# Performance work log

Measured on AMD Instinct MI355X. Metric: run time of the kernel, lower is better.

The kernel has to match this reference:

```python
import jax, jax.numpy as jnp
import numpy as np

N_NODES = 50000
N_FEAT = 32
HIDDEN = 64
K_HOPS = 3
N_EDGES = 800000
BN_EPS = 1e-5


def setup_inputs() -> dict:
    key = jax.random.key(0)
    ks = jax.random.split(key, 16)
    x = jax.random.normal(ks[0], (N_NODES, N_FEAT), jnp.float32)
    edge_index = jax.random.randint(ks[1], (2, N_EDGES), 0, N_NODES, jnp.int32)
    edge_weight = jax.random.uniform(ks[2], (N_EDGES,), jnp.float32, minval=0.1, maxval=1.0)
    fin = N_FEAT + HIDDEN  # DCRNN cell concatenates [X, H]
    s = 1.0 / np.sqrt(fin)
    Wz = jax.random.uniform(ks[3], (2, K_HOPS, fin, HIDDEN), jnp.float32, -s, s)
    Wr = jax.random.uniform(ks[4], (2, K_HOPS, fin, HIDDEN), jnp.float32, -s, s)
    Wh = jax.random.uniform(ks[5], (2, K_HOPS, fin, HIDDEN), jnp.float32, -s, s)
    bz = jax.random.uniform(ks[6], (HIDDEN,), jnp.float32, -s, s)
    br = jax.random.uniform(ks[7], (HIDDEN,), jnp.float32, -s, s)
    bh = jax.random.uniform(ks[8], (HIDDEN,), jnp.float32, -s, s)
    g = 1.0 / np.sqrt(HIDDEN)
    gcn_w = jax.random.uniform(ks[9], (HIDDEN, HIDDEN), jnp.float32, -g, g)
    gcn_b = jax.random.uniform(ks[10], (HIDDEN,), jnp.float32, -g, g)
    bn_gamma = jnp.ones((HIDDEN,), jnp.float32)
    bn_beta = jnp.zeros((HIDDEN,), jnp.float32)
    lin_w = jax.random.uniform(ks[11], (HIDDEN, 1), jnp.float32, -g, g)
    lin_b = jax.random.uniform(ks[12], (1,), jnp.float32, -g, g)
    return dict(x=x, edge_index=edge_index, edge_weight=edge_weight,
                Wz=Wz, bz=bz, Wr=Wr, br=br, Wh=Wh, bh=bh,
                gcn_w=gcn_w, gcn_b=gcn_b, bn_gamma=bn_gamma, bn_beta=bn_beta,
                lin_w=lin_w, lin_b=lin_b)


def _dconv(X, W, b, row, col, ew, do_inv, di_inv, n):
    # Diffusion conv: H = sum_k T_out^k(X) @ W[0,k] + T_in^k(X) @ W[1,k] + b
    # T_out: propagate along edges (source -> target), out-degree normalized
    # T_in : propagate along reversed edges, in-degree normalized
    H = X @ W[0, 0] + X @ W[1, 0]
    Tx_o = X
    Tx_i = X
    w_out = (ew * do_inv[row])[:, None]  # [E,1]
    w_in = (ew * di_inv[col])[:, None]   # [E,1]
    for k in range(1, W.shape[1]):
        Tx_o = jax.ops.segment_sum(w_out * Tx_o[row], col, num_segments=n)
        Tx_i = jax.ops.segment_sum(w_in * Tx_i[col], row, num_segments=n)
        H = H + Tx_o @ W[0, k] + Tx_i @ W[1, k]
    return H + b


def reference(x, edge_index, edge_weight, Wz, bz, Wr, br, Wh, bh,
              gcn_w, gcn_b, bn_gamma, bn_beta, lin_w, lin_b):
    n = x.shape[0]
    row, col = edge_index[0], edge_index[1]
    # weighted degrees (as in DConv's dense-adjacency degree computation)
    deg_out = jax.ops.segment_sum(edge_weight, row, num_segments=n)
    deg_in = jax.ops.segment_sum(edge_weight, col, num_segments=n)
    do_inv = jnp.where(deg_out > 0, 1.0 / deg_out, 0.0)
    di_inv = jnp.where(deg_in > 0, 1.0 / deg_in, 0.0)

    # --- DCRNN cell (GRU with diffusion convs), hidden state starts at zero ---
    H0 = jnp.zeros((n, Wz.shape[-1]), x.dtype)
    XH = jnp.concatenate([x, H0], axis=1)
    Z = jax.nn.sigmoid(_dconv(XH, Wz, bz, row, col, edge_weight, do_inv, di_inv, n))
    R = jax.nn.sigmoid(_dconv(XH, Wr, br, row, col, edge_weight, do_inv, di_inv, n))
    XHR = jnp.concatenate([x, H0 * R], axis=1)
    H_tilde = jnp.tanh(_dconv(XHR, Wh, bh, row, col, edge_weight, do_inv, di_inv, n))
    H = Z * H0 + (1.0 - Z) * H_tilde  # [N, HIDDEN]

    # --- GCNConv(H, edge_index) with unit edge weights + self loops, sym norm ---
    xw = H @ gcn_w
    ones_e = jnp.ones((row.shape[0],), x.dtype)
    deg = jax.ops.segment_sum(ones_e, col, num_segments=n) + 1.0  # + self loop
    dis = jnp.where(deg > 0, jax.lax.rsqrt(deg), 0.0)
    norm = (dis[row] * dis[col])[:, None]
    y = jax.ops.segment_sum(norm * xw[row], col, num_segments=n) + (dis * dis)[:, None] * xw
    y = y + gcn_b

    # ReLU -> BatchNorm1d (batch statistics, biased var) -> Dropout(identity/eval) -> Linear
    y = jax.nn.relu(y)
    mean = jnp.mean(y, axis=0)
    var = jnp.mean(jnp.square(y - mean), axis=0)
    y = (y - mean) * jax.lax.rsqrt(var + BN_EPS) * bn_gamma + bn_beta
    out = y @ lin_w + lin_b  # [N, 1]
    return out
```

## Files before the change

### kernel.cpp

```cpp
#include <hip/hip_runtime.h>
#include <hip/hip_fp16.h>
#include <math.h>


#define BN_EPS 1e-5f
#define CAPB 6
#define CAP  64
#define ITEMS 2048
#define KI 8
#define REGCAP 5120

typedef _Float16 v8h __attribute__((ext_vector_type(8)));
typedef float v4f __attribute__((ext_vector_type(4)));

__global__ __launch_bounds__(256) void k_sort1(
    const int* __restrict__ row, const int* __restrict__ col,
    const float* __restrict__ ew,
    unsigned long long* __restrict__ bufC, unsigned long long* __restrict__ bufR,
    unsigned* __restrict__ gcnt, int E, int nbk, int reg) {
    __shared__ unsigned hist[256], scanb[256], cur[256], runb[256];
    __shared__ unsigned long long outb[ITEMS];
    int t = threadIdx.x;
    int s = (blockIdx.x >= nbk) ? 1 : 0;
    int blk = blockIdx.x - s * nbk;
    int e0 = blk * ITEMS;
    int vcnt = E - e0; if (vcnt > ITEMS) vcnt = ITEMS;
    hist[t] = 0;
    __syncthreads();
    for (int k = 0; k < KI; ++k) {
        int e = e0 + k * 256 + t;
        if (e < E) {
            int key = s ? row[e] : col[e];
            atomicAdd(&hist[key >> 8], 1u);
        }
    }
    __syncthreads();
    scanb[t] = hist[t];
    __syncthreads();
    for (int off = 1; off < 256; off <<= 1) {
        unsigned v = (t >= off) ? scanb[t - off] : 0u;
        __syncthreads();
        scanb[t] += v;
        __syncthreads();
    }
    unsigned excl = scanb[t] - hist[t];
    __syncthreads();
    scanb[t] = excl;
    cur[t] = excl;
    runb[t] = (unsigned)(t * reg) + atomicAdd(&gcnt[s * 256 + t], hist[t]);
    __syncthreads();
    for (int k = 0; k < KI; ++k) {
        int e = e0 + k * 256 + t;
        if (e < E) {
            int key, oth;
            if (s) { key = row[e]; oth = col[e]; }
            else   { key = col[e]; oth = row[e]; }
            unsigned hw = (unsigned)__half_as_ushort(__float2half(ew[e]));
            unsigned long long it = ((unsigned long long)(unsigned)key << 32)
                                  | ((unsigned)oth << 16) | hw;
            unsigned r = atomicAdd(&cur[key >> 8], 1u);
            outb[r] = it;
        }
    }
    __syncthreads();
    unsigned long long* buf = s ? bufR : bufC;
    for (int k = 0; k < KI; ++k) {
        int idx = k * 256 + t;
        if (idx < vcnt) {
            unsigned long long it = outb[idx];
            unsigned d = (unsigned)(it >> 40) & 255u;
            buf[(size_t)runb[d] + ((unsigned)idx - scanb[d])] = it;
        }
    }
}

__global__ __launch_bounds__(256) void k_sort2(
    const unsigned long long* __restrict__ buf, const unsigned* __restrict__ gcnt,
    unsigned* __restrict__ ent, int* __restrict__ cnt, int N, int reg) {
    __shared__ unsigned hist[256], scanb[256], cur[256];
    __shared__ unsigned outp[REGCAP];
    __shared__ unsigned char outl[REGCAP];
    int t = threadIdx.x;
    int d0 = blockIdx.x;
    const unsigned long long* src = buf + (size_t)d0 * reg;
    int cin = (int)gcnt[d0]; if (cin > REGCAP) cin = REGCAP;
    hist[t] = 0;
    __syncthreads();
    for (int i = t; i < cin; i += 256) {
        unsigned l = (unsigned)(src[i] >> 32) & 255u;
        atomicAdd(&hist[l], 1u);
    }
    __syncthreads();
    scanb[t] = hist[t];
    __syncthreads();
    for (int off = 1; off < 256; off <<= 1) {
        unsigned v = (t >= off) ? scanb[t - off] : 0u;
        __syncthreads();
        scanb[t] += v;
        __syncthreads();
    }
    unsigned excl = scanb[t] - hist[t];
    __syncthreads();
    scanb[t] = excl;
    cur[t] = excl;
    int node0 = d0 << 8;
    if (node0 + t < N) cnt[node0 + t] = (int)hist[t];
    __syncthreads();
    for (int i = t; i < cin; i += 256) {
        unsigned long long it = src[i];
        unsigned l = (unsigned)(it >> 32) & 255u;
        unsigned r = atomicAdd(&cur[l], 1u);
        outp[r] = (unsigned)it;
        outl[r] = (unsigned char)l;
    }
    __syncthreads();
    for (int i = t; i < cin; i += 256) {
        unsigned l = outl[i];
        int slot = i - (int)scanb[l];
        int node = node0 + (int)l;
        if (slot < CAP && node < N)
            ent[((size_t)node << CAPB) + slot] = outp[i];
    }
}

__device__ inline float ent_w(unsigned e) {
    return __half2float(__ushort_as_half((unsigned short)(e & 0xffffu)));
}

__global__ void k_degs(const unsigned* __restrict__ ent_col, const unsigned* __restrict__ ent_row,
                       const int* __restrict__ cnt_col, const int* __restrict__ cnt_row,
                       float* __restrict__ do_inv, float* __restrict__ di_inv,
                       float* __restrict__ dis, int N) {
    int i = blockIdx.x * blockDim.x + threadIdx.x;
    if (i >= N) return;
    float s = 0.f;
    int c = min(cnt_row[i], CAP);
    const unsigned* er = ent_row + ((size_t)i << CAPB);
    for (int j = 0; j < c; ++j) s += ent_w(er[j]);
    do_inv[i] = s > 0.f ? 1.f / s : 0.f;
    s = 0.f;
    c = min(cnt_col[i], CAP);
    const unsigned* ec = ent_col + ((size_t)i << CAPB);
    for (int j = 0; j < c; ++j) s += ent_w(ec[j]);
    di_inv[i] = s > 0.f ? 1.f / s : 0.f;
    dis[i] = rsqrtf((float)cnt_col[i] + 1.0f);
}

__global__ void k_cvt_x(const float* __restrict__ xf, __half* __restrict__ xh, int n2) {
    int t = blockIdx.x * blockDim.x + threadIdx.x;
    if (t >= n2) return;
    float2 v = *(const float2*)(xf + 2 * (size_t)t);
    __half2 h; h.x = __float2half(v.x); h.y = __float2half(v.y);
    *(__half2*)(xh + 2 * (size_t)t) = h;
}

__global__ void k_hop(const unsigned* __restrict__ ent_col, const unsigned* __restrict__ ent_row,
                      const int* __restrict__ cnt_col, const int* __restrict__ cnt_row,
                      const __half* __restrict__ So, const __half* __restrict__ Si,
                      const float* __restrict__ do_inv, const float* __restrict__ di_inv,
                      __half* __restrict__ Do, __half* __restrict__ Di, int N) {
    int t = blockIdx.x * blockDim.x + threadIdx.x;
    int f = t & 31;
    int p = t >> 5;
    if (p >= 2 * N) return;
    const unsigned* ent; const __half* S; const float* inv; __half* D;
    int d, cnt;
    if (p < N) { d = p;     ent = ent_col; S = So; inv = do_inv; D = Do; cnt = min(cnt_col[d], CAP); }
    else       { d = p - N; ent = ent_row; S = Si; inv = di_inv; D = Di; cnt = min(cnt_row[d], CAP); }
    ent += ((size_t)d << CAPB);
    float acc = 0.f;
    int j = 0;
    for (; j + 7 < cnt; j += 8) {
        unsigned e0 = ent[j],     e1 = ent[j + 1], e2 = ent[j + 2], e3 = ent[j + 3];
        unsigned e4 = ent[j + 4], e5 = ent[j + 5], e6 = ent[j + 6], e7 = ent[j + 7];
        int s0 = e0 >> 16, s1 = e1 >> 16, s2 = e2 >> 16, s3 = e3 >> 16;
        int s4 = e4 >> 16, s5 = e5 >> 16, s6 = e6 >> 16, s7 = e7 >> 16;
        float i0 = inv[s0], i1 = inv[s1], i2 = inv[s2], i3 = inv[s3];
        float i4 = inv[s4], i5 = inv[s5], i6 = inv[s6], i7 = inv[s7];
        float v0 = __half2float(S[(size_t)s0 * 32 + f]);
        float v1 = __half2float(S[(size_t)s1 * 32 + f]);
        float v2 = __half2float(S[(size_t)s2 * 32 + f]);
        float v3 = __half2float(S[(size_t)s3 * 32 + f]);
        float v4 = __half2float(S[(size_t)s4 * 32 + f]);
        float v5 = __half2float(S[(size_t)s5 * 32 + f]);
        float v6 = __half2float(S[(size_t)s6 * 32 + f]);
        float v7 = __half2float(S[(size_t)s7 * 32 + f]);
        acc += ent_w(e0) * i0 * v0 + ent_w(e1) * i1 * v1
             + ent_w(e2) * i2 * v2 + ent_w(e3) * i3 * v3
             + ent_w(e4) * i4 * v4 + ent_w(e5) * i5 * v5
             + ent_w(e6) * i6 * v6 + ent_w(e7) * i7 * v7;
    }
    for (; j + 3 < cnt; j += 4) {
        unsigned e0 = ent[j],     e1 = ent[j + 1];
        unsigned e2 = ent[j + 2], e3 = ent[j + 3];
        int s0 = e0 >> 16, s1 = e1 >> 16, s2 = e2 >> 16, s3 = e3 >> 16;
        float i0 = inv[s0], i1 = inv[s1], i2 = inv[s2], i3 = inv[s3];
        float v0 = __half2float(S[(size_t)s0 * 32 + f]);
        float v1 = __half2float(S[(size_t)s1 * 32 + f]);
        float v2 = __half2float(S[(size_t)s2 * 32 + f]);
        float v3 = __half2float(S[(size_t)s3 * 32 + f]);
        acc += ent_w(e0) * i0 * v0 + ent_w(e1) * i1 * v1
             + ent_w(e2) * i2 * v2 + ent_w(e3) * i3 * v3;
    }
    for (; j < cnt; ++j) {
        unsigned e0 = ent[j];
        int s0 = e0 >> 16;
        acc += ent_w(e0) * inv[s0] * __half2float(S[(size_t)s0 * 32 + f]);
    }
    D[(size_t)d * 32 + f] = __float2half(acc);
}

__global__ void k_wprep(const float* __restrict__ Wz, const float* __restrict__ Wh,
                        const float* __restrict__ gcn_w,
                        __half* __restrict__ wzT, __half* __restrict__ whT,
                        __half* __restrict__ gwT) {
    int t = blockIdx.x * blockDim.x + threadIdx.x;
    if (t < 64 * 160) {
        int c = t / 160, k = t % 160;
        int blk = k >> 5, r = k & 31;
        float vz, vh;
        if (blk == 0) {
            vz = Wz[r * 64 + c] + Wz[(288 + r) * 64 + c];
            vh = Wh[r * 64 + c] + Wh[(288 + r) * 64 + c];
        } else {
            int kk = (blk + 1) >> 1, dd = (blk + 1) & 1;
            int off = ((dd * 3 + kk) * 96 + r) * 64 + c;
            vz = Wz[off]; vh = Wh[off];
        }
        wzT[t] = __float2half(vz);
        whT[t] = __float2half(vh);
    }
    if (t < 64 * 64) {
        int c = t >> 6, k = t & 63;
        gwT[t] = __float2half(gcn_w[k * 64 + c]);
    }
}

__device__ inline v8h ldh8(const __half* p) { return *(const v8h*)p; }

__global__ __launch_bounds__(256) void k_zh_mfma(
    const __half* __restrict__ xh, const __half* __restrict__ t1o,
    const __half* __restrict__ t1i, const __half* __restrict__ t2o,
    const __half* __restrict__ t2i,
    const __half* __restrict__ wzT, const __half* __restrict__ whT,
    const __half* __restrict__ gwT,
    const float* __restrict__ bz, const float* __restrict__ bh,
    const float* __restrict__ dis, float* __restrict__ xws, int N) {
    __shared__ _Float16 Hl[16 * 72];
    int lane = threadIdx.x & 63;
    int wv = threadIdx.x >> 6;
    int q = lane >> 4, m = lane & 15;
    int c = wv * 16 + m;
    int ko = q * 8;

    const __half* wz = wzT + c * 160 + ko;
    const __half* wh = whT + c * 160 + ko;
    v8h bz0 = ldh8(wz),       bh0 = ldh8(wh);
    v8h bz1 = ldh8(wz + 32),  bh1 = ldh8(wh + 32);
    v8h bz2 = ldh8(wz + 64),  bh2 = ldh8(wh + 64);
    v8h bz3 = ldh8(wz + 96),  bh3 = ldh8(wh + 96);
    v8h bz4 = ldh8(wz + 128), bh4 = ldh8(wh + 128);
    v8h g0 = ldh8(gwT + c * 64 + ko);
    v8h g1 = ldh8(gwT + c * 64 + 32 + ko);
    float bzc = bz[c], bhc = bh[c];

    int T = (N + 15) >> 4;
    for (int t = blockIdx.x; t < T; t += gridDim.x) {
        int n0 = t << 4;
        int nn = n0 + m; if (nn > N - 1) nn = N - 1;
        size_t off = (size_t)nn * 32 + ko;
        v8h a0 = ldh8(xh + off);
        v8h a1 = ldh8(t1o + off);
        v8h a2 = ldh8(t1i + off);
        v8h a3 = ldh8(t2o + off);
        v8h a4 = ldh8(t2i + off);
        v4f az = {0.f, 0.f, 0.f, 0.f}, ah = {0.f, 0.f, 0.f, 0.f};
        az = __builtin_amdgcn_mfma_f32_16x16x32_f16(a0, bz0, az, 0, 0, 0);
        ah = __builtin_amdgcn_mfma_f32_16x16x32_f16(a0, bh0, ah, 0, 0, 0);
        az = __builtin_amdgcn_mfma_f32_16x16x32_f16(a1, bz1, az, 0, 0, 0);
        ah = __builtin_amdgcn_mfma_f32_16x16x32_f16(a1, bh1, ah, 0, 0, 0);
        az = __builtin_amdgcn_mfma_f32_16x16x32_f16(a2, bz2, az, 0, 0, 0);
        ah = __builtin_amdgcn_mfma_f32_16x16x32_f16(a2, bh2, ah, 0, 0, 0);
        az = __builtin_amdgcn_mfma_f32_16x16x32_f16(a3, bz3, az, 0, 0, 0);
        ah = __builtin_amdgcn_mfma_f32_16x16x32_f16(a3, bh3, ah, 0, 0, 0);
        az = __builtin_amdgcn_mfma_f32_16x16x32_f16(a4, bz4, az, 0, 0, 0);
        ah = __builtin_amdgcn_mfma_f32_16x16x32_f16(a4, bh4, ah, 0, 0, 0);

#pragma unroll
        for (int i = 0; i < 4; ++i) {
            float zv = 1.f / (1.f + expf(-(az[i] + bzc)));
            float hv = (1.f - zv) * tanhf(ah[i] + bhc);
            Hl[(q * 4 + i) * 72 + c] = (_Float16)hv;
        }
        __syncthreads();
        v8h ha0 = *(const v8h*)&Hl[m * 72 + ko];
        v8h ha1 = *(const v8h*)&Hl[m * 72 + 32 + ko];
        v4f bacc = {0.f, 0.f, 0.f, 0.f};
        bacc = __builtin_amdgcn_mfma_f32_16x16x32_f16(ha0, g0, bacc, 0, 0, 0);
        bacc = __builtin_amdgcn_mfma_f32_16x16x32_f16(ha1, g1, bacc, 0, 0, 0);
#pragma unroll
        for (int i = 0; i < 4; ++i) {
            int node = n0 + q * 4 + i;
            if (node < N) xws[(size_t)node * 64 + c] = dis[node] * bacc[i];
        }
        __syncthreads();
    }
}

__global__ __launch_bounds__(256) void k_gcn16(
    const unsigned* __restrict__ ent_col, const int* __restrict__ cnt_col,
    const float* __restrict__ dis, const float* __restrict__ xws,
    const float* __restrict__ gcn_b,
    float* __restrict__ y, float* __restrict__ stats, int N) {
    __shared__ float red[2][256];
    int t = threadIdx.x;
    int ch = t & 15;
    int grp = t >> 4;
    int s = blockIdx.x & 3;
    int cg = s * 16 + ch;
    float bl = gcn_b[cg];
    int bi = blockIdx.x >> 2;
    int nblk = gridDim.x >> 2;
    float sa = 0.f, s2a = 0.f;
    for (int d = bi * 16 + grp; d < N; d += nblk * 16) {
        float sum = xws[(size_t)d * 64 + cg];
        const unsigned* ent = ent_col + ((size_t)d << CAPB);
        int cnt = min(cnt_col[d], CAP);
        int j = 0;
        for (; j + 7 < cnt; j += 8) {
            unsigned e0 = ent[j],     e1 = ent[j + 1], e2 = ent[j + 2], e3 = ent[j + 3];
            unsigned e4 = ent[j + 4], e5 = ent[j + 5], e6 = ent[j + 6], e7 = ent[j + 7];
            float v0 = xws[(size_t)(e0 >> 16) * 64 + cg];
            float v1 = xws[(size_t)(e1 >> 16) * 64 + cg];
            float v2 = xws[(size_t)(e2 >> 16) * 64 + cg];
            float v3 = xws[(size_t)(e3 >> 16) * 64 + cg];
            float v4 = xws[(size_t)(e4 >> 16) * 64 + cg];
            float v5 = xws[(size_t)(e5 >> 16) * 64 + cg];
            float v6 = xws[(size_t)(e6 >> 16) * 64 + cg];
            float v7 = xws[(size_t)(e7 >> 16) * 64 + cg];
            sum += (v0 + v1 + v2 + v3) + (v4 + v5 + v6 + v7);
        }
        for (; j + 3 < cnt; j += 4) {
            unsigned e0 = ent[j],     e1 = ent[j + 1];
            unsigned e2 = ent[j + 2], e3 = ent[j + 3];
            float v0 = xws[(size_t)(e0 >> 16) * 64 + cg];
            float v1 = xws[(size_t)(e1 >> 16) * 64 + cg];
            float v2 = xws[(size_t)(e2 >> 16) * 64 + cg];
            float v3 = xws[(size_t)(e3 >> 16) * 64 + cg];
            sum += v0 + v1 + v2 + v3;
        }
        for (; j < cnt; ++j) {
            unsigned e0 = ent[j];
            sum += xws[(size_t)(e0 >> 16) * 64 + cg];
        }
        float v = dis[d] * sum + bl;
        v = v > 0.f ? v : 0.f;
        y[(size_t)d * 64 + cg] = v;
        sa += v; s2a += v * v;
    }
    red[0][t] = sa;
    red[1][t] = s2a;
    __syncthreads();
    if (t < 16) {
        float ts = 0.f, ts2 = 0.f;
        for (int k = t; k < 256; k += 16) { ts += red[0][k]; ts2 += red[1][k]; }
        atomicAdd(&stats[s * 16 + t], ts);
        atomicAdd(&stats[64 + s * 16 + t], ts2);
    }
}

__global__ void k_final(const float* __restrict__ y, const float* __restrict__ stats,
                        const float* __restrict__ gma, const float* __restrict__ bta,
                        const float* __restrict__ lw, const float* __restrict__ lb,
                        float* __restrict__ out, int N) {
    int lane = threadIdx.x & 63;
    int wave = (blockIdx.x * blockDim.x + threadIdx.x) >> 6;
    if (wave >= N) return;
    float invN = 1.0f / (float)N;
    float mean = stats[lane] * invN;
    float var  = stats[64 + lane] * invN - mean * mean;
    float istd = rsqrtf(var + BN_EPS);
    float v = y[(size_t)wave * 64 + lane];
    float t = (v - mean) * istd * gma[lane] + bta[lane];
    float p = t * lw[lane];
    for (int off = 32; off > 0; off >>= 1)
        p += __shfl_down(p, off, 64);
    if (lane == 0) out[wave] = p + lb[0];
}

extern "C" void kernel_launch(void* const* d_in, const int* in_sizes, int n_in,
                              void* d_out, int out_size, void* d_ws, size_t ws_size,
                              hipStream_t stream) {
    const float* x     = (const float*)d_in[0];
    const int*   ei    = (const int*)d_in[1];
    const float* ew    = (const float*)d_in[2];
    const float* Wz    = (const float*)d_in[3];
    const float* bz    = (const float*)d_in[4];
    const float* Wh    = (const float*)d_in[7];
    const float* bhv   = (const float*)d_in[8];
    const float* gcn_w = (const float*)d_in[9];
    const float* gcn_b = (const float*)d_in[10];
    const float* gma   = (const float*)d_in[11];
    const float* bta   = (const float*)d_in[12];
    const float* lw    = (const float*)d_in[13];
    const float* lb    = (const float*)d_in[14];
    float* out = (float*)d_out;

    const int N = in_sizes[0] / 32;
    const int E = in_sizes[2];
    const int* row = ei;
    const int* col = ei + E;

    float* ws      = (float*)d_ws;
    int*   cnt_col = (int*)ws;
    int*   cnt_row = (int*)(ws + (size_t)N);
    unsigned* gcnt = (unsigned*)(ws + 2 * (size_t)N);
    float* stats   = ws + 2 * (size_t)N + 512;
    size_t Z0      = 2 * (size_t)N + 640;
    float* dis     = ws + Z0;
    float* do_inv  = ws + Z0 + (size_t)N;
    float* di_inv  = ws + Z0 + 2 * (size_t)N;
    __half* xh     = (__half*)(ws + Z0 + 3 * (size_t)N);
    __half* txo1   = (__half*)(ws + Z0 + 19 * (size_t)N);
    __half* txi1   = (__half*)(ws + Z0 + 35 * (size_t)N);
    __half* txo2   = (__half*)(ws + Z0 + 51 * (size_t)N);
    __half* txi2   = (__half*)(ws + Z0 + 67 * (size_t)N);
    unsigned* ent_col = (unsigned*)(ws + Z0 + 83 * (size_t)N);
    unsigned* ent_row = ent_col + ((size_t)N << CAPB);
    float* xws     = (float*)ent_row;
    float* ybuf    = (float*)txo1;
    __half* wzT    = (__half*)(ws + Z0 + 211 * (size_t)N);
    __half* whT    = wzT + 64 * 160;
    __half* gwT    = whT + 64 * 160;

    unsigned long long* bufC = (unsigned long long*)ent_row;
    unsigned long long* bufR = (unsigned long long*)txo1;

    size_t zero_bytes = (2 * (size_t)N + 640) * sizeof(float);
    hipMemsetAsync(d_ws, 0, zero_bytes, stream);

    int NB = (N + 255) / 256;
    int nbk = (E + ITEMS - 1) / ITEMS;
    int ndig = (N + 255) / 256;
    k_cvt_x<<<(16 * N + 255) / 256, 256, 0, stream>>>(x, xh, 16 * N);
    k_wprep<<<40, 256, 0, stream>>>(Wz, Wh, gcn_w, wzT, whT, gwT);
    k_sort1<<<2 * nbk, 256, 0, stream>>>(row, col, ew, bufC, bufR, gcnt, E, nbk, REGCAP);
    k_sort2<<<ndig, 256, 0, stream>>>(bufC, gcnt,       ent_col, cnt_col, N, REGCAP);
    k_sort2<<<ndig, 256, 0, stream>>>(bufR, gcnt + 256, ent_row, cnt_row, N, REGCAP);
    k_degs <<<NB, 256, 0, stream>>>(ent_col, ent_row, cnt_col, cnt_row,
                                    do_inv, di_inv, dis, N);

    int bhop = (2 * N * 32 + 255) / 256;
    k_hop<<<bhop, 256, 0, stream>>>(ent_col, ent_row, cnt_col, cnt_row,
                                    xh, xh, do_inv, di_inv, txo1, txi1, N);
    k_hop<<<bhop, 256, 0, stream>>>(ent_col, ent_row, cnt_col, cnt_row,
                                    txo1, txi1, do_inv, di_inv, txo2, txi2, N);

    k_zh_mfma<<<1024, 256, 0, stream>>>(xh, txo1, txi1, txo2, txi2,
                                        wzT, whT, gwT, bz, bhv, dis, xws, N);

    k_gcn16<<<1600, 256, 0, stream>>>(ent_col, cnt_col, dis, xws,
                                      gcn_b, ybuf, stats, N);
    k_final<<<(N + 3) / 4, 256, 0, stream>>>(ybuf, stats, gma, bta, lw, lb, out, N);
}
```

Measured before the change: 291.0 us.

## Aggregate GCN neighbors before the weight matmul, gathering fp16 hidden states

```diff
diff --git a/kernel.cpp b/kernel.cpp
--- a/kernel.cpp
+++ b/kernel.cpp
@@ -243,10 +243,8 @@
     const __half* __restrict__ t1i, const __half* __restrict__ t2o,
     const __half* __restrict__ t2i,
     const __half* __restrict__ wzT, const __half* __restrict__ whT,
-    const __half* __restrict__ gwT,
     const float* __restrict__ bz, const float* __restrict__ bh,
-    const float* __restrict__ dis, float* __restrict__ xws, int N) {
-    __shared__ _Float16 Hl[16 * 72];
+    const float* __restrict__ dis, __half* __restrict__ Hd, int N) {
     int lane = threadIdx.x & 63;
     int wv = threadIdx.x >> 6;
     int q = lane >> 4, m = lane & 15;
@@ -260,8 +258,6 @@
     v8h bz2 = ldh8(wz + 64),  bh2 = ldh8(wh + 64);
     v8h bz3 = ldh8(wz + 96),  bh3 = ldh8(wh + 96);
     v8h bz4 = ldh8(wz + 128), bh4 = ldh8(wh + 128);
-    v8h g0 = ldh8(gwT + c * 64 + ko);
-    v8h g1 = ldh8(gwT + c * 64 + 32 + ko);
     float bzc = bz[c], bhc = bh[c];
 
     int T = (N + 15) >> 4;
@@ -290,82 +286,104 @@
         for (int i = 0; i < 4; ++i) {
             float zv = 1.f / (1.f + expf(-(az[i] + bzc)));
             float hv = (1.f - zv) * tanhf(ah[i] + bhc);
-            Hl[(q * 4 + i) * 72 + c] = (_Float16)hv;
-        }
-        __syncthreads();
-        v8h ha0 = *(const v8h*)&Hl[m * 72 + ko];
-        v8h ha1 = *(const v8h*)&Hl[m * 72 + 32 + ko];
-        v4f bacc = {0.f, 0.f, 0.f, 0.f};
-        bacc = __builtin_amdgcn_mfma_f32_16x16x32_f16(ha0, g0, bacc, 0, 0, 0);
-        bacc = __builtin_amdgcn_mfma_f32_16x16x32_f16(ha1, g1, bacc, 0, 0, 0);
+            int node = n0 + q * 4 + i;
+            if (node < N) Hd[(size_t)node * 64 + c] = __float2half(dis[node] * hv);
+        }
+    }
+}
+
+__global__ __launch_bounds__(256) void k_agg(
+    const unsigned* __restrict__ ent_col, const int* __restrict__ cnt_col,
+    const float* __restrict__ dis, const __half* __restrict__ Hd,
+    float* __restrict__ P, int N) {
+    int t = blockIdx.x * blockDim.x + threadIdx.x;
+    int ch = t & 63;
+    int d = t >> 6;
+    if (d >= N) return;
+    const unsigned* ent = ent_col + ((size_t)d << CAPB);
+    int cnt = min(cnt_col[d], CAP);
+    float acc = __half2float(Hd[(size_t)d * 64 + ch]);
+    int j = 0;
+    for (; j + 7 < cnt; j += 8) {
+        unsigned e0 = ent[j],     e1 = ent[j + 1], e2 = ent[j + 2], e3 = ent[j + 3];
+        unsigned e4 = ent[j + 4], e5 = ent[j + 5], e6 = ent[j + 6], e7 = ent[j + 7];
+        float v0 = __half2float(Hd[(size_t)(e0 >> 16) * 64 + ch]);
+        float v1 = __half2float(Hd[(size_t)(e1 >> 16) * 64 + ch]);
+        float v2 = __half2float(Hd[(size_t)(e2 >> 16) * 64 + ch]);
+        float v3 = __half2float(Hd[(size_t)(e3 >> 16) * 64 + ch]);
+        float v4 = __half2float(Hd[(size_t)(e4 >> 16) * 64 + ch]);
+        float v5 = __half2float(Hd[(size_t)(e5 >> 16) * 64 + ch]);
+        float v6 = __half2float(Hd[(size_t)(e6 >> 16) * 64 + ch]);
+        float v7 = __half2float(Hd[(size_t)(e7 >> 16) * 64 + ch]);
+        acc += (v0 + v1 + v2 + v3) + (v4 + v5 + v6 + v7);
+    }
+    for (; j + 3 < cnt; j += 4) {
+        unsigned e0 = ent[j],     e1 = ent[j + 1];
+        unsigned e2 = ent[j + 2], e3 = ent[j + 3];
+        float v0 = __half2float(Hd[(size_t)(e0 >> 16) * 64 + ch]);
+        float v1 = __half2float(Hd[(size_t)(e1 >> 16) * 64 + ch]);
+        float v2 = __half2float(Hd[(size_t)(e2 >> 16) * 64 + ch]);
+        float v3 = __half2float(Hd[(size_t)(e3 >> 16) * 64 + ch]);
+        acc += v0 + v1 + v2 + v3;
+    }
+    for (; j < cnt; ++j) {
+        acc += __half2float(Hd[(size_t)(ent[j] >> 16) * 64 + ch]);
+    }
+    P[(size_t)d * 64 + ch] = dis[d] * acc;
+}
+
+__global__ __launch_bounds__(256) void k_gcn2(
+    const float* __restrict__ P, const __half* __restrict__ gwT,
+    const float* __restrict__ gcn_b,
+    float* __restrict__ y, float* __restrict__ stats, int N) {
+    __shared__ float red[2][256];
+    int lane = threadIdx.x & 63;
+    int wv = threadIdx.x >> 6;
+    int q = lane >> 4, m = lane & 15;
+    int c = wv * 16 + m;
+    int ko = q * 8;
+    v8h g0 = ldh8(gwT + c * 64 + ko);
+    v8h g1 = ldh8(gwT + c * 64 + 32 + ko);
+    float bl = gcn_b[c];
+    float sa = 0.f, s2a = 0.f;
+    int T = (N + 15) >> 4;
+    for (int t = blockIdx.x; t < T; t += gridDim.x) {
+        int n0 = t << 4;
+        int nn = n0 + m; if (nn > N - 1) nn = N - 1;
+        const float* pr = P + (size_t)nn * 64;
+        v4f p0 = *(const v4f*)(pr + ko);
+        v4f p1 = *(const v4f*)(pr + ko + 4);
+        v4f p2 = *(const v4f*)(pr + 32 + ko);
+        v4f p3 = *(const v4f*)(pr + 32 + ko + 4);
+        v8h a0, a1;
+#pragma unroll
+        for (int j = 0; j < 4; ++j) {
+            a0[j] = (_Float16)p0[j]; a0[4 + j] = (_Float16)p1[j];
+            a1[j] = (_Float16)p2[j]; a1[4 + j] = (_Float16)p3[j];
+        }
+        v4f acc = {0.f, 0.f, 0.f, 0.f};
+        acc = __builtin_amdgcn_mfma_f32_16x16x32_f16(a0, g0, acc, 0, 0, 0);
+        acc = __builtin_amdgcn_mfma_f32_16x16x32_f16(a1, g1, acc, 0, 0, 0);
 #pragma unroll
         for (int i = 0; i < 4; ++i) {
             int node = n0 + q * 4 + i;
-            if (node < N) xws[(size_t)node * 64 + c] = dis[node] * bacc[i];
-        }
-        __syncthreads();
-    }
-}
-
-__global__ __launch_bounds__(256) void k_gcn16(
-    const unsigned* __restrict__ ent_col, const int* __restrict__ cnt_col,
-    const float* __restrict__ dis, const float* __restrict__ xws,
-    const float* __restrict__ gcn_b,
-    float* __restrict__ y, float* __restrict__ stats, int N) {
-    __shared__ float red[2][256];
-    int t = threadIdx.x;
-    int ch = t & 15;
-    int grp = t >> 4;
-    int s = blockIdx.x & 3;
-    int cg = s * 16 + ch;
-    float bl = gcn_b[cg];
-    int bi = blockIdx.x >> 2;
-    int nblk = gridDim.x >> 2;
-    float sa = 0.f, s2a = 0.f;
-    for (int d = bi * 16 + grp; d < N; d += nblk * 16) {
-        float sum = xws[(size_t)d * 64 + cg];
-        const unsigned* ent = ent_col + ((size_t)d << CAPB);
-        int cnt = min(cnt_col[d], CAP);
-        int j = 0;
-        for (; j + 7 < cnt; j += 8) {
-            unsigned e0 = ent[j],     e1 = ent[j + 1], e2 = ent[j + 2], e3 = ent[j + 3];
-            unsigned e4 = ent[j + 4], e5 = ent[j + 5], e6 = ent[j + 6], e7 = ent[j + 7];
-            float v0 = xws[(size_t)(e0 >> 16) * 64 + cg];
-            float v1 = xws[(size_t)(e1 >> 16) * 64 + cg];
-            float v2 = xws[(size_t)(e2 >> 16) * 64 + cg];
-            float v3 = xws[(size_t)(e3 >> 16) * 64 + cg];
-            float v4 = xws[(size_t)(e4 >> 16) * 64 + cg];
-            float v5 = xws[(size_t)(e5 >> 16) * 64 + cg];
-            float v6 = xws[(size_t)(e6 >> 16) * 64 + cg];
-            float v7 = xws[(size_t)(e7 >> 16) * 64 + cg];
-            sum += (v0 + v1 + v2 + v3) + (v4 + v5 + v6 + v7);
-        }
-        for (; j + 3 < cnt; j += 4) {
-            unsigned e0 = ent[j],     e1 = ent[j + 1];
-            unsigned e2 = ent[j + 2], e3 = ent[j + 3];
-            float v0 = xws[(size_t)(e0 >> 16) * 64 + cg];
-            float v1 = xws[(size_t)(e1 >> 16) * 64 + cg];
-            float v2 = xws[(size_t)(e2 >> 16) * 64 + cg];
-            float v3 = xws[(size_t)(e3 >> 16) * 64 + cg];
-            sum += v0 + v1 + v2 + v3;
-        }
-        for (; j < cnt; ++j) {
-            unsigned e0 = ent[j];
-            sum += xws[(size_t)(e0 >> 16) * 64 + cg];
-        }
-        float v = dis[d] * sum + bl;
-        v = v > 0.f ? v : 0.f;
-        y[(size_t)d * 64 + cg] = v;
-        sa += v; s2a += v * v;
-    }
-    red[0][t] = sa;
-    red[1][t] = s2a;
-    __syncthreads();
-    if (t < 16) {
-        float ts = 0.f, ts2 = 0.f;
-        for (int k = t; k < 256; k += 16) { ts += red[0][k]; ts2 += red[1][k]; }
-        atomicAdd(&stats[s * 16 + t], ts);
-        atomicAdd(&stats[64 + s * 16 + t], ts2);
+            if (node < N) {
+                float v = acc[i] + bl;
+                v = v > 0.f ? v : 0.f;
+                y[(size_t)node * 64 + c] = v;
+                sa += v; s2a += v * v;
+            }
+        }
+    }
+    red[0][threadIdx.x] = sa;
+    red[1][threadIdx.x] = s2a;
+    __syncthreads();
+    if (q == 0) {
+        int t0 = threadIdx.x;
+        float ts  = red[0][t0] + red[0][t0 + 16] + red[0][t0 + 32] + red[0][t0 + 48];
+        float ts2 = red[1][t0] + red[1][t0 + 16] + red[1][t0 + 32] + red[1][t0 + 48];
+        atomicAdd(&stats[c], ts);
+        atomicAdd(&stats[64 + c], ts2);
     }
 }
 
@@ -427,14 +445,15 @@
     __half* txi2   = (__half*)(ws + Z0 + 67 * (size_t)N);
     unsigned* ent_col = (unsigned*)(ws + Z0 + 83 * (size_t)N);
     unsigned* ent_row = ent_col + ((size_t)N << CAPB);
-    float* xws     = (float*)ent_row;
-    float* ybuf    = (float*)txo1;
     __half* wzT    = (__half*)(ws + Z0 + 211 * (size_t)N);
     __half* whT    = wzT + 64 * 160;
     __half* gwT    = whT + 64 * 160;
 
     unsigned long long* bufC = (unsigned long long*)ent_row;
     unsigned long long* bufR = (unsigned long long*)txo1;
+    __half* Hd = (__half*)ent_row;
+    float*  P  = (float*)xh;
+    float*  yb = (float*)ent_col;
 
     size_t zero_bytes = (2 * (size_t)N + 640) * sizeof(float);
     hipMemsetAsync(d_ws, 0, zero_bytes, stream);
@@ -457,9 +476,9 @@
                                     txo1, txi1, do_inv, di_inv, txo2, txi2, N);
 
     k_zh_mfma<<<1024, 256, 0, stream>>>(xh, txo1, txi1, txo2, txi2,
-                                        wzT, whT, gwT, bz, bhv, dis, xws, N);
-
-    k_gcn16<<<1600, 256, 0, stream>>>(ent_col, cnt_col, dis, xws,
-                                      gcn_b, ybuf, stats, N);
-    k_final<<<(N + 3) / 4, 256, 0, stream>>>(ybuf, stats, gma, bta, lw, lb, out, N);
-}
+                                        wzT, whT, bz, bhv, dis, Hd, N);
+
+    k_agg<<<(64 * N + 255) / 256, 256, 0, stream>>>(ent_col, cnt_col, dis, Hd, P, N);
+    k_gcn2<<<1024, 256, 0, stream>>>(P, gwT, gcn_b, yb, stats, N);
+    k_final<<<(N + 3) / 4, 256, 0, stream>>>(yb, stats, gma, bta, lw, lb, out, N);
+}
```

Measured after the change: 298.2 us. 1.02x slower.
